# Kernel tuning notes

Measured on AMD Instinct MI355X. Metric: run time of the kernel, lower is better.

## Reference

```python
import jax, jax.numpy as jnp
import numpy as np

KERNEL = (9, 9, 9)  # box-filter window
KSIZE = KERNEL[0] * KERNEL[1] * KERNEL[2]  # 729
GAMMA = 1.0


def _box_sum(x):
    # x: [B, C, D, H, W] -> channel-sum then 9x9x9 sliding-window sum (SAME pad),
    # exactly matching F.conv3d with an all-ones [1, C, 9,9,9] kernel, pad=4.
    s = jnp.sum(x, axis=1, keepdims=True)  # [B,1,D,H,W]
    return jax.lax.reduce_window(
        s, jnp.asarray(0.0, s.dtype), jax.lax.add,
        window_dimensions=(1, 1) + KERNEL,
        window_strides=(1, 1, 1, 1, 1),
        padding='SAME')


def setup_inputs() -> dict:
    key = jax.random.key(0)
    k1, k2, k3 = jax.random.split(key, 3)
    shape = (2, 1, 160, 160, 160)
    return {
        'input': jax.random.normal(k1, shape, dtype=jnp.float32),
        'target': jax.random.normal(k2, shape, dtype=jnp.float32),
        'flow': jax.random.normal(k3, shape, dtype=jnp.float32),
    }


def reference(input, target, flow):
    # normalize target from (-1, 1) to (0, 1)
    target = (target + 1.0) * 0.5
    w = jax.nn.sigmoid(flow) ** GAMMA  # voxel-wise confidence weight

    T_sum = _box_sum(target)
    I_sum = _box_sum(input)
    TT_sum = _box_sum(target * target)
    II_sum = _box_sum(input * input)
    IT_sum = _box_sum(input * target)

    Ihat = I_sum / KSIZE
    That = T_sum / KSIZE
    cross = IT_sum - Ihat * T_sum - That * I_sum + That * Ihat * KSIZE
    T_var = TT_sum - 2.0 * That * T_sum + That * That * KSIZE
    I_var = II_sum - 2.0 * Ihat * I_sum + Ihat * Ihat * KSIZE

    cc = cross * cross * w / (T_var * I_var + 1e-5)
    return -1.0 * jnp.mean(cc)
```

## Files before the change

kernel.cpp:

```cpp
#include <hip/hip_runtime.h>


constexpr int NB = 2;
constexpr int ND = 160;
constexpr int NH = 160;
constexpr int NW = 160;
constexpr int TH = 16;
constexpr int TW = 16;
constexpr int DCHUNK = 32;
constexpr int NDCH = ND / DCHUNK;
constexpr float INV_K = 1.0f / 729.0f;
constexpr double INV_COUNT = 1.0 / (double(NB) * ND * NH * NW);

__device__ __forceinline__ void compute_plane(
    const float* __restrict__ in, const float* __restrict__ tg,
    int b, int dp, int h0, int w0, int tid,
    float* __restrict__ inT, float* __restrict__ tgT,
    float* __restrict__ tmp5, float* __restrict__ Pbuf)
{
    if (tid < 144) {
        int r = tid / 6;
        int q = tid - r * 6;
        int gh = h0 - 4 + r;
        int gw = w0 - 4 + q * 4;
        float4 iv = make_float4(0.f, 0.f, 0.f, 0.f);
        float4 tv = make_float4(0.f, 0.f, 0.f, 0.f);
        if (((unsigned)gh < (unsigned)NH) && ((unsigned)gw < (unsigned)NW)) {
            long base = ((long)((b * ND + dp) * NH + gh)) * NW + gw;
            iv = *reinterpret_cast<const float4*>(in + base);
            float4 rv = *reinterpret_cast<const float4*>(tg + base);
            tv.x = fmaf(rv.x, 0.5f, 0.5f);
            tv.y = fmaf(rv.y, 0.5f, 0.5f);
            tv.z = fmaf(rv.z, 0.5f, 0.5f);
            tv.w = fmaf(rv.w, 0.5f, 0.5f);
        }
        reinterpret_cast<float4*>(inT)[r * 6 + q] = iv;
        reinterpret_cast<float4*>(tgT)[r * 6 + q] = tv;
    }
    __syncthreads();

    {
        int pos = tid;
        #pragma unroll
        for (int rep = 0; rep < 2; ++rep) {
            if (pos < 384) {
                int r = pos >> 4, wo = pos & 15;
                const float* ir = inT + r * 24 + wo;
                const float* tr = tgT + r * 24 + wo;
                float s0 = 0.f, s1 = 0.f, s2 = 0.f, s3 = 0.f, s4 = 0.f;
                #pragma unroll
                for (int k = 0; k < 9; ++k) {
                    float ivv = ir[k];
                    float t = tr[k];
                    s0 += t;
                    s1 += ivv;
                    s2 = fmaf(t, t, s2);
                    s3 = fmaf(ivv, ivv, s3);
                    s4 = fmaf(ivv, t, s4);
                }
                int o = r * 16 + wo;
                tmp5[0 * 384 + o] = s0;
                tmp5[1 * 384 + o] = s1;
                tmp5[2 * 384 + o] = s2;
                tmp5[3 * 384 + o] = s3;
                tmp5[4 * 384 + o] = s4;
            }
            pos += 256;
        }
    }
    __syncthreads();

    if (tid < 80) {
        int f = tid >> 4, w = tid & 15;
        const float* basep = tmp5 + f * 384 + w;
        float s = 0.f;
        #pragma unroll
        for (int r = 0; r < 8; ++r) s += basep[r * 16];
        #pragma unroll
        for (int ho = 0; ho < 16; ++ho) {
            s += basep[(ho + 8) * 16];
            Pbuf[f * 256 + ho * 16 + w] = s;
            s -= basep[ho * 16];
        }
    }
    __syncthreads();
}

__global__ void __launch_bounds__(256)
cc3d_main(const float* __restrict__ in, const float* __restrict__ tg,
          const float* __restrict__ fl, double* __restrict__ acc_out)
{
    __shared__ float inT[24 * 24];
    __shared__ float tgT[24 * 24];
    __shared__ float tmp5[5 * 24 * 16];
    __shared__ float Pbuf[5 * 16 * 16];
    __shared__ float red[4];

    const int tid = threadIdx.x;
    const int w0 = blockIdx.x * TW;
    const int h0 = blockIdx.y * TH;
    const int bz = blockIdx.z;
    const int b  = bz / NDCH;
    const int d0 = (bz - b * NDCH) * DCHUNK;

    float ring[45];
    #pragma unroll
    for (int i = 0; i < 45; ++i) ring[i] = 0.f;
    float S[5] = {0.f, 0.f, 0.f, 0.f, 0.f};
    float acc = 0.f;

    #pragma unroll
    for (int l = 0; l < 8; ++l) {
        int dp = d0 - 4 + l;
        bool valid = (dp >= 0);
        if (valid) compute_plane(in, tg, b, dp, h0, w0, tid, inT, tgT, tmp5, Pbuf);
        #pragma unroll
        for (int f = 0; f < 5; ++f) {
            float pv = valid ? Pbuf[f * 256 + tid] : 0.f;
            ring[f * 9 + l] = pv;
            S[f] += pv;
        }
    }

    for (int jbase = 0; jbase < DCHUNK; jbase += 9) {
        #pragma unroll
        for (int jj = 0; jj < 9; ++jj) {
            int j = jbase + jj;
            if (j < DCHUNK) {
                int dout = d0 + j;
                int dp = dout + 4;
                bool valid = (dp < ND);
                if (valid) compute_plane(in, tg, b, dp, h0, w0, tid, inT, tgT, tmp5, Pbuf);
                const int slot = (jj + 8) % 9;
                #pragma unroll
                for (int f = 0; f < 5; ++f) {
                    float pn = valid ? Pbuf[f * 256 + tid] : 0.f;
                    S[f] += pn - ring[f * 9 + slot];
                    ring[f * 9 + slot] = pn;
                }
                int hh = tid >> 4, ww = tid & 15;
                long fidx = ((long)((b * ND + dout) * NH + (h0 + hh))) * NW + (w0 + ww);
                float x = fl[fidx];
                float wgt = 1.0f / (1.0f + __expf(-x));
                float Ts = S[0], Is = S[1], TTs = S[2], IIs = S[3], ITs = S[4];
                float Ihat = Is * INV_K;
                float That = Ts * INV_K;
                float cross = ITs - Ihat * Ts - That * Is + That * Ihat * 729.0f;
                float T_var = TTs - 2.0f * That * Ts + That * That * 729.0f;
                float I_var = IIs - 2.0f * Ihat * Is + Ihat * Ihat * 729.0f;
                float cc = cross * cross * wgt / (T_var * I_var + 1e-5f);
                acc += cc;
            }
        }
    }

    #pragma unroll
    for (int off = 32; off > 0; off >>= 1) acc += __shfl_down(acc, off);
    if ((tid & 63) == 0) red[tid >> 6] = acc;
    __syncthreads();
    if (tid == 0) {
        double v = (double)red[0] + (double)red[1] + (double)red[2] + (double)red[3];
        atomicAdd(acc_out, v);
    }
}

__global__ void cc3d_finalize(const double* __restrict__ acc, float* __restrict__ out)
{
    out[0] = (float)(-(acc[0] * INV_COUNT));
}

extern "C" void kernel_launch(void* const* d_in, const int* in_sizes, int n_in,
                              void* d_out, int out_size, void* d_ws, size_t ws_size,
                              hipStream_t stream)
{
    const float* in = (const float*)d_in[0];
    const float* tg = (const float*)d_in[1];
    const float* fl = (const float*)d_in[2];
    float* out = (float*)d_out;
    double* acc = (double*)d_ws;

    hipMemsetAsync(d_ws, 0, sizeof(double), stream);

    dim3 grid(NW / TW, NH / TH, NB * NDCH);
    cc3d_main<<<grid, dim3(256), 0, stream>>>(in, tg, fl, acc);
    cc3d_finalize<<<1, 1, 0, stream>>>(acc, out);
}
```

Baseline: 186.0 us.

## Prefetch next depth plane into registers and halve depth chunk size

Splits plane processing into a global load issue, a shared-memory staging step, and the reduction steps, so the next plane's loads are in flight while the current plane is reduced. The depth chunk shrinks from 32 to 16 planes, doubling the grid for more parallelism at the cost of more halo planes recomputed per block. Shared-memory strides are padded (392, 264) to reduce bank conflicts, and index arithmetic moves to 32-bit ints. The flow load is issued before the barriers as well.

```diff
diff --git a/kernel.cpp b/kernel.cpp
--- a/kernel.cpp
+++ b/kernel.cpp
@@ -7,26 +7,28 @@
 constexpr int NW = 160;
 constexpr int TH = 16;
 constexpr int TW = 16;
-constexpr int DCHUNK = 32;
+constexpr int DCHUNK = 16;
 constexpr int NDCH = ND / DCHUNK;
+constexpr int NPL = DCHUNK + 8;
+constexpr int FS5 = 392;
+constexpr int PFS = 264;
 constexpr float INV_K = 1.0f / 729.0f;
 constexpr double INV_COUNT = 1.0 / (double(NB) * ND * NH * NW);
 
-__device__ __forceinline__ void compute_plane(
+__device__ __forceinline__ void issue_load(
     const float* __restrict__ in, const float* __restrict__ tg,
     int b, int dp, int h0, int w0, int tid,
-    float* __restrict__ inT, float* __restrict__ tgT,
-    float* __restrict__ tmp5, float* __restrict__ Pbuf)
-{
-    if (tid < 144) {
+    float4& iv, float4& tv)
+{
+    iv = make_float4(0.f, 0.f, 0.f, 0.f);
+    tv = make_float4(0.f, 0.f, 0.f, 0.f);
+    if (tid < 144 && ((unsigned)dp < (unsigned)ND)) {
         int r = tid / 6;
         int q = tid - r * 6;
         int gh = h0 - 4 + r;
         int gw = w0 - 4 + q * 4;
-        float4 iv = make_float4(0.f, 0.f, 0.f, 0.f);
-        float4 tv = make_float4(0.f, 0.f, 0.f, 0.f);
         if (((unsigned)gh < (unsigned)NH) && ((unsigned)gw < (unsigned)NW)) {
-            long base = ((long)((b * ND + dp) * NH + gh)) * NW + gw;
+            int base = ((b * ND + dp) * NH + gh) * NW + gw;
             iv = *reinterpret_cast<const float4*>(in + base);
             float4 rv = *reinterpret_cast<const float4*>(tg + base);
             tv.x = fmaf(rv.x, 0.5f, 0.5f);
@@ -34,56 +36,79 @@
             tv.z = fmaf(rv.z, 0.5f, 0.5f);
             tv.w = fmaf(rv.w, 0.5f, 0.5f);
         }
-        reinterpret_cast<float4*>(inT)[r * 6 + q] = iv;
-        reinterpret_cast<float4*>(tgT)[r * 6 + q] = tv;
-    }
-    __syncthreads();
-
-    {
-        int pos = tid;
-        #pragma unroll
-        for (int rep = 0; rep < 2; ++rep) {
-            if (pos < 384) {
-                int r = pos >> 4, wo = pos & 15;
-                const float* ir = inT + r * 24 + wo;
-                const float* tr = tgT + r * 24 + wo;
-                float s0 = 0.f, s1 = 0.f, s2 = 0.f, s3 = 0.f, s4 = 0.f;
-                #pragma unroll
-                for (int k = 0; k < 9; ++k) {
-                    float ivv = ir[k];
-                    float t = tr[k];
-                    s0 += t;
-                    s1 += ivv;
-                    s2 = fmaf(t, t, s2);
-                    s3 = fmaf(ivv, ivv, s3);
-                    s4 = fmaf(ivv, t, s4);
-                }
-                int o = r * 16 + wo;
-                tmp5[0 * 384 + o] = s0;
-                tmp5[1 * 384 + o] = s1;
-                tmp5[2 * 384 + o] = s2;
-                tmp5[3 * 384 + o] = s3;
-                tmp5[4 * 384 + o] = s4;
-            }
-            pos += 256;
-        }
-    }
-    __syncthreads();
-
+    }
+}
+
+__device__ __forceinline__ void stage(int tid, const float4& iv, const float4& tv,
+                                      float* __restrict__ inT, float* __restrict__ tgT)
+{
+    if (tid < 144) {
+        reinterpret_cast<float4*>(inT)[tid] = iv;
+        reinterpret_cast<float4*>(tgT)[tid] = tv;
+    }
+}
+
+__device__ __forceinline__ void step2(int tid, const float* __restrict__ inT,
+                                      const float* __restrict__ tgT,
+                                      float* __restrict__ tmp5)
+{
+    int pos = tid;
+    #pragma unroll
+    for (int rep = 0; rep < 2; ++rep) {
+        if (pos < 384) {
+            int r = pos >> 4, wo = pos & 15;
+            const float* ir = inT + r * 24 + wo;
+            const float* tr = tgT + r * 24 + wo;
+            float s0 = 0.f, s1 = 0.f, s2 = 0.f, s3 = 0.f, s4 = 0.f;
+            #pragma unroll
+            for (int k = 0; k < 9; ++k) {
+                float ivv = ir[k];
+                float t = tr[k];
+                s0 += t;
+                s1 += ivv;
+                s2 = fmaf(t, t, s2);
+                s3 = fmaf(ivv, ivv, s3);
+                s4 = fmaf(ivv, t, s4);
+            }
+            int o = r * 16 + wo;
+            tmp5[0 * FS5 + o] = s0;
+            tmp5[1 * FS5 + o] = s1;
+            tmp5[2 * FS5 + o] = s2;
+            tmp5[3 * FS5 + o] = s3;
+            tmp5[4 * FS5 + o] = s4;
+        }
+        pos += 256;
+    }
+}
+
+__device__ __forceinline__ void step3(int tid, const float* __restrict__ tmp5,
+                                      float* __restrict__ Pbuf)
+{
     if (tid < 80) {
         int f = tid >> 4, w = tid & 15;
-        const float* basep = tmp5 + f * 384 + w;
+        const float* basep = tmp5 + f * FS5 + w;
         float s = 0.f;
         #pragma unroll
         for (int r = 0; r < 8; ++r) s += basep[r * 16];
         #pragma unroll
         for (int ho = 0; ho < 16; ++ho) {
             s += basep[(ho + 8) * 16];
-            Pbuf[f * 256 + ho * 16 + w] = s;
+            Pbuf[f * PFS + ho * 16 + w] = s;
             s -= basep[ho * 16];
         }
     }
-    __syncthreads();
+}
+
+__device__ __forceinline__ float cc_value(const float S[5], float flv)
+{
+    float wgt = 1.0f / (1.0f + __expf(-flv));
+    float Ts = S[0], Is = S[1], TTs = S[2], IIs = S[3], ITs = S[4];
+    float Ihat = Is * INV_K;
+    float That = Ts * INV_K;
+    float cross = ITs - Ihat * Ts - That * Is + That * Ihat * 729.0f;
+    float T_var = TTs - 2.0f * That * Ts + That * That * 729.0f;
+    float I_var = IIs - 2.0f * Ihat * Is + Ihat * Ihat * 729.0f;
+    return cross * cross * wgt / (T_var * I_var + 1e-5f);
 }
 
 __global__ void __launch_bounds__(256)
@@ -92,8 +117,8 @@
 {
     __shared__ float inT[24 * 24];
     __shared__ float tgT[24 * 24];
-    __shared__ float tmp5[5 * 24 * 16];
-    __shared__ float Pbuf[5 * 16 * 16];
+    __shared__ float tmp5[5 * FS5];
+    __shared__ float Pbuf[5 * PFS];
     __shared__ float red[4];
 
     const int tid = threadIdx.x;
@@ -102,6 +127,7 @@
     const int bz = blockIdx.z;
     const int b  = bz / NDCH;
     const int d0 = (bz - b * NDCH) * DCHUNK;
+    const int hh = tid >> 4, ww = tid & 15;
 
     float ring[45];
     #pragma unroll
@@ -109,47 +135,73 @@
     float S[5] = {0.f, 0.f, 0.f, 0.f, 0.f};
     float acc = 0.f;
 
-    #pragma unroll
-    for (int l = 0; l < 8; ++l) {
-        int dp = d0 - 4 + l;
-        bool valid = (dp >= 0);
-        if (valid) compute_plane(in, tg, b, dp, h0, w0, tid, inT, tgT, tmp5, Pbuf);
+    float4 iv, tv;
+    issue_load(in, tg, b, d0 - 4, h0, w0, tid, iv, tv);
+
+    #pragma unroll
+    for (int l = 0; l < 9; ++l) {
+        stage(tid, iv, tv, inT, tgT);
+        float4 niv, ntv;
+        issue_load(in, tg, b, d0 - 4 + l + 1, h0, w0, tid, niv, ntv);
+        float flv = 0.f;
+        if (l == 8) {
+            int fidx = ((b * ND + d0) * NH + (h0 + hh)) * NW + (w0 + ww);
+            flv = fl[fidx];
+        }
+        __syncthreads();
+        step2(tid, inT, tgT, tmp5);
+        __syncthreads();
+        step3(tid, tmp5, Pbuf);
+        __syncthreads();
+        if (l < 8) {
+            #pragma unroll
+            for (int f = 0; f < 5; ++f) {
+                float pv = Pbuf[f * PFS + tid];
+                ring[f * 9 + l] = pv;
+                S[f] += pv;
+            }
+        } else {
+            #pragma unroll
+            for (int f = 0; f < 5; ++f) {
+                float pn = Pbuf[f * PFS + tid];
+                S[f] += pn - ring[f * 9 + 8];
+                ring[f * 9 + 8] = pn;
+            }
+            acc += cc_value(S, flv);
+        }
+        iv = niv; tv = ntv;
+    }
+
+    for (int lb = 9; lb < 27; lb += 9) {
         #pragma unroll
-        for (int f = 0; f < 5; ++f) {
-            float pv = valid ? Pbuf[f * 256 + tid] : 0.f;
-            ring[f * 9 + l] = pv;
-            S[f] += pv;
-        }
-    }
-
-    for (int jbase = 0; jbase < DCHUNK; jbase += 9) {
-        #pragma unroll
-        for (int jj = 0; jj < 9; ++jj) {
-            int j = jbase + jj;
-            if (j < DCHUNK) {
-                int dout = d0 + j;
-                int dp = dout + 4;
-                bool valid = (dp < ND);
-                if (valid) compute_plane(in, tg, b, dp, h0, w0, tid, inT, tgT, tmp5, Pbuf);
-                const int slot = (jj + 8) % 9;
+        for (int li = 0; li < 9; ++li) {
+            const int l = lb + li;
+            if (l < NPL) {
+                stage(tid, iv, tv, inT, tgT);
+                float4 niv, ntv;
+                if (l < NPL - 1) {
+                    issue_load(in, tg, b, d0 - 4 + l + 1, h0, w0, tid, niv, ntv);
+                } else {
+                    niv = make_float4(0.f, 0.f, 0.f, 0.f);
+                    ntv = niv;
+                }
+                int dout = d0 + (l - 8);
+                int fidx = ((b * ND + dout) * NH + (h0 + hh)) * NW + (w0 + ww);
+                float flv = fl[fidx];
+                __syncthreads();
+                step2(tid, inT, tgT, tmp5);
+                __syncthreads();
+                step3(tid, tmp5, Pbuf);
+                __syncthreads();
+                const int slot = li;
                 #pragma unroll
                 for (int f = 0; f < 5; ++f) {
-                    float pn = valid ? Pbuf[f * 256 + tid] : 0.f;
+                    float pn = Pbuf[f * PFS + tid];
                     S[f] += pn - ring[f * 9 + slot];
                     ring[f * 9 + slot] = pn;
                 }
-                int hh = tid >> 4, ww = tid & 15;
-                long fidx = ((long)((b * ND + dout) * NH + (h0 + hh))) * NW + (w0 + ww);
-                float x = fl[fidx];
-                float wgt = 1.0f / (1.0f + __expf(-x));
-                float Ts = S[0], Is = S[1], TTs = S[2], IIs = S[3], ITs = S[4];
-                float Ihat = Is * INV_K;
-                float That = Ts * INV_K;
-                float cross = ITs - Ihat * Ts - That * Is + That * Ihat * 729.0f;
-                float T_var = TTs - 2.0f * That * Ts + That * That * 729.0f;
-                float I_var = IIs - 2.0f * Ihat * Is + Ihat * Ihat * 729.0f;
-                float cc = cross * cross * wgt / (T_var * I_var + 1e-5f);
-                acc += cc;
+                acc += cc_value(S, flv);
+                iv = niv; tv = ntv;
             }
         }
     }
```

Result: slower. 195.7 us (+5.2%).
